# Kernel tuning notes

Measured on AMD Instinct MI355X. Metric: run time of the kernel, lower is better.

## Reference

```python
import jax, jax.numpy as jnp
import numpy as np

B, T, D, H = 4, 2048, 1024, 16
DK = D // H
LN_EPS = 1e-5


def setup_inputs() -> dict:
    key = jax.random.key(0)
    ks = jax.random.split(key, 12)
    s = 1.0 / np.sqrt(D)
    inp = {
        'x': jax.random.normal(ks[0], (B, T, D), jnp.float32),
        'Wq': jax.random.normal(ks[1], (D, D), jnp.float32) * s,
        'bq': jnp.zeros((D,), jnp.float32),
        'Wk': jax.random.normal(ks[2], (D, D), jnp.float32) * s,
        'bk': jnp.zeros((D,), jnp.float32),
        'Wv': jax.random.normal(ks[3], (D, D), jnp.float32) * s,
        'bv': jnp.zeros((D,), jnp.float32),
        'Wo': jax.random.normal(ks[4], (D, D), jnp.float32) * s,
        'bo': jnp.zeros((D,), jnp.float32),
        'ln_g': jnp.ones((D,), jnp.float32),
        'ln_b': jnp.zeros((D,), jnp.float32),
    }
    return inp


def reference(x, Wq, bq, Wk, bk, Wv, bv, Wo, bo, ln_g, ln_b):
    b, t, d = x.shape
    scale = jnp.sqrt(jnp.asarray(DK, x.dtype))
    # QKV projections -> [b, h, t, dk]
    q = (x @ Wq + bq).reshape(b, t, H, DK).transpose(0, 2, 1, 3)
    k = (x @ Wk + bk).reshape(b, t, H, DK).transpose(0, 2, 1, 3)
    v = (x @ Wv + bv).reshape(b, t, H, DK).transpose(0, 2, 1, 3)
    scores = jnp.einsum('bhqd,bhkd->bhqk', q, k) / scale  # [b,h,t,t]
    mask = jnp.tril(jnp.ones((t, t), x.dtype))[None, None]  # [1,1,t,t]
    neg = jnp.finfo(x.dtype).min
    scores = jnp.where(mask == 0, neg, scores)
    attn = jax.nn.softmax(scores, axis=-1)
    # mask-renormalize (as in the torch module)
    attn = attn * mask
    denom = attn.sum(-1, keepdims=True)
    attn = jnp.where(denom > 0, attn / denom, jnp.zeros_like(attn))
    ctx = jnp.einsum('bhqk,bhkd->bhqd', attn, v)  # [b,h,t,dk]
    ctx = ctx.transpose(0, 2, 1, 3).reshape(b, t, d)
    out = ctx @ Wo + bo
    y = out + x  # residual
    mu = y.mean(-1, keepdims=True)
    var = ((y - mu) ** 2).mean(-1, keepdims=True)
    return (y - mu) / jnp.sqrt(var + LN_EPS) * ln_g + ln_b
```

## Files before the change

### kernel.cpp

```cpp
#include <hip/hip_runtime.h>


using u16 = unsigned short;
using u32 = unsigned int;
typedef _Float16 f16x8 __attribute__((ext_vector_type(8)));
typedef float f32x4 __attribute__((ext_vector_type(4)));
typedef unsigned short u16x8 __attribute__((ext_vector_type(8)));

template <bool B> struct BoolTag { static constexpr bool v = B; };

__device__ inline u16 f2h_bits(float f) {
    _Float16 h = (_Float16)f;
    return __builtin_bit_cast(u16, h);
}

__device__ __forceinline__ void gload16(const void* g, void* l) {
    __builtin_amdgcn_global_load_lds(
        (const __attribute__((address_space(1))) void*)g,
        (__attribute__((address_space(3))) void*)l, 16, 0, 0);
}

__global__ __launch_bounds__(256) void convert_x_kernel(const float* __restrict__ x,
                                                        u16* __restrict__ xb) {
    size_t i = ((size_t)blockIdx.x * 256 + threadIdx.x) * 8;
    float4 a = *(const float4*)(x + i);
    float4 b = *(const float4*)(x + i + 4);
    u16x8 o;
    o[0] = f2h_bits(a.x); o[1] = f2h_bits(a.y); o[2] = f2h_bits(a.z); o[3] = f2h_bits(a.w);
    o[4] = f2h_bits(b.x); o[5] = f2h_bits(b.y); o[6] = f2h_bits(b.z); o[7] = f2h_bits(b.w);
    *(u16x8*)(xb + i) = o;
}

__global__ __launch_bounds__(256) void convert_wt_kernel(const float* __restrict__ W,
                                                         u16* __restrict__ Wt) {
    __shared__ float ts[64][68];
    const int k0 = blockIdx.x * 64, n0 = blockIdx.y * 64;
    const int tid = threadIdx.x, rr = tid >> 3, c = tid & 7;
#pragma unroll
    for (int p = 0; p < 2; p++) {
        int k = p * 32 + rr;
        float4 u = *(const float4*)(W + (size_t)(k0 + k) * 1024 + n0 + c * 8);
        float4 w = *(const float4*)(W + (size_t)(k0 + k) * 1024 + n0 + c * 8 + 4);
        *(float4*)&ts[k][c * 8] = u;
        *(float4*)&ts[k][c * 8 + 4] = w;
    }
    __syncthreads();
#pragma unroll
    for (int p = 0; p < 2; p++) {
        int n = p * 32 + rr;
        u16 o[8];
#pragma unroll
        for (int j = 0; j < 8; j++) o[j] = f2h_bits(ts[c * 8 + j][n]);
        *(u16x8*)(Wt + (size_t)(n0 + n) * 1024 + k0 + c * 8) = *(u16x8*)o;
    }
}

template <int MODE>
__global__ __launch_bounds__(512) void gemm256_kernel(
    const u16* __restrict__ A, const u16* __restrict__ Wt,
    const float* __restrict__ b0, const float* __restrict__ b1,
    const float* __restrict__ b2, u16* __restrict__ qo, u16* __restrict__ ko,
    u16* __restrict__ vo, float* __restrict__ outf,
    const float* __restrict__ xres) {
    constexpr int NBY = (MODE == 0) ? 12 : 4;
    __shared__ u16 As[3][128 * 64];
    __shared__ u16 Bs[3][256 * 64];

    const int bid = blockIdx.x;
    const int cpx = (MODE == 0) ? 96 : 32;
    const int swz = (bid & 7) * cpx + (bid >> 3);
    const int bx = swz / NBY, by = swz % NBY;
    const size_t row0 = (size_t)bx * 128;
    const size_t col0 = (size_t)by * 256;

    const int tid = threadIdx.x, lane = tid & 63;
    const int wid = tid >> 6, wm = wid >> 2, wn = wid & 3;
    const int l15 = lane & 15, lg = lane >> 4;
    const int rr = tid >> 3, c8 = tid & 7;
    const int scw = (c8 ^ (rr & 7)) * 8;

    f32x4 acc[4][4] = {};

    auto stage_half = [&](int kt, u16* dA, u16* dB, int h) {
        const int k0 = kt * 64;
        if (h == 0) {
            gload16(A + (row0 + rr) * 1024 + k0 + scw, dA + tid * 8);
            gload16(Wt + (col0 + rr) * 1024 + k0 + scw, dB + tid * 8);
            gload16(Wt + (col0 + 64 + rr) * 1024 + k0 + scw, dB + (512 + tid) * 8);
        } else {
            gload16(A + (row0 + 64 + rr) * 1024 + k0 + scw, dA + (512 + tid) * 8);
            gload16(Wt + (col0 + 128 + rr) * 1024 + k0 + scw, dB + (1024 + tid) * 8);
            gload16(Wt + (col0 + 192 + rr) * 1024 + k0 + scw, dB + (1536 + tid) * 8);
        }
    };

    auto ldops = [&](const u16* bA, const u16* bB, int kcv, f16x8* Af, f16x8* Bf) {
        const int swo = ((kcv * 4 + lg) ^ (l15 & 7)) * 8;
#pragma unroll
        for (int n = 0; n < 4; n++)
            Bf[n] = *(const f16x8*)(bB + (wn * 64 + n * 16 + l15) * 64 + swo);
#pragma unroll
        for (int m = 0; m < 4; m++)
            Af[m] = *(const f16x8*)(bA + (wm * 64 + m * 16 + l15) * 64 + swo);
    };

    auto domfma = [&](const f16x8* Af, const f16x8* Bf) {
        __builtin_amdgcn_s_setprio(1);
#pragma unroll
        for (int m = 0; m < 4; m++)
#pragma unroll
            for (int n = 0; n < 4; n++)
                acc[m][n] = __builtin_amdgcn_mfma_f32_16x16x32_f16(
                    Af[m], Bf[n], acc[m][n], 0, 0, 0);
        __builtin_amdgcn_s_setprio(0);
    };

    u16 *pA = &As[0][0], *pnA = &As[1][0], *ppA = &As[2][0];
    u16 *pB = &Bs[0][0], *pnB = &Bs[1][0], *ppB = &Bs[2][0];

    stage_half(0, pA, pB, 0);
    stage_half(0, pA, pB, 1);
    stage_half(1, pnA, pnB, 0);
    stage_half(1, pnA, pnB, 1);
    asm volatile("s_waitcnt vmcnt(6)" ::: "memory");
    __builtin_amdgcn_sched_barrier(0);
    __builtin_amdgcn_s_barrier();

#pragma unroll 1
    for (int t = 0; t < 16; t++) {
        f16x8 af[4], bf[4];
        ldops(pA, pB, 0, af, bf);
        if (t < 14) stage_half(t + 2, ppA, ppB, 0);
        __builtin_amdgcn_sched_barrier(0);
        __builtin_amdgcn_s_barrier();
        asm volatile("s_waitcnt lgkmcnt(0)" ::: "memory");
        __builtin_amdgcn_sched_barrier(0);
        domfma(af, bf);
        __builtin_amdgcn_sched_barrier(0);
        __builtin_amdgcn_s_barrier();
        ldops(pA, pB, 1, af, bf);
        if (t < 14) stage_half(t + 2, ppA, ppB, 1);
        if (t < 14)       asm volatile("s_waitcnt vmcnt(6)" ::: "memory");
        else if (t == 14) asm volatile("s_waitcnt vmcnt(0)" ::: "memory");
        __builtin_amdgcn_sched_barrier(0);
        __builtin_amdgcn_s_barrier();
        asm volatile("s_waitcnt lgkmcnt(0)" ::: "memory");
        __builtin_amdgcn_sched_barrier(0);
        domfma(af, bf);
        __builtin_amdgcn_sched_barrier(0);
        if (t < 15) {
            __builtin_amdgcn_s_barrier();
            u16* tp;
            tp = pA; pA = pnA; pnA = ppA; ppA = tp;
            tp = pB; pB = pnB; pnB = ppB; ppB = tp;
        }
    }

    if (MODE == 0) {
        const int zsel = by >> 2;
        u16* ob = zsel == 0 ? qo : (zsel == 1 ? ko : vo);
        const float* bias = zsel == 0 ? b0 : (zsel == 1 ? b1 : b2);
        const float qs = zsel == 0 ? 0.18033688f : 1.0f;
#pragma unroll
        for (int m = 0; m < 4; m++) {
#pragma unroll
            for (int n = 0; n < 4; n++) {
                size_t col = col0 + wn * 64 + n * 16 + l15;
                size_t colz = col & 1023;
                float bb = bias[colz];
#pragma unroll
                for (int r = 0; r < 4; r++) {
                    size_t row = row0 + wm * 64 + m * 16 + lg * 4 + r;
                    ob[row * 1024 + colz] = f2h_bits((acc[m][n][r] + bb) * qs);
                }
            }
        }
    } else {
#pragma unroll
        for (int m = 0; m < 4; m++) {
#pragma unroll
            for (int n = 0; n < 4; n++) {
                size_t col = col0 + wn * 64 + n * 16 + l15;
                float bb = b0[col];
#pragma unroll
                for (int r = 0; r < 4; r++) {
                    size_t row = row0 + wm * 64 + m * 16 + lg * 4 + r;
                    size_t idx = row * 1024 + col;
                    outf[idx] = acc[m][n][r] + bb + xres[idx];
                }
            }
        }
    }
}

__global__ __launch_bounds__(256) void transpose_v_kernel(const u16* __restrict__ V,
                                                          u16* __restrict__ Vt) {
    __shared__ u16 ts[64][72];
    const int bh = blockIdx.y;
    const int b = bh >> 4, h = bh & 15;
    const int t0 = blockIdx.x * 64;
    const int tid = threadIdx.x, rr = tid >> 3, c = tid & 7;
#pragma unroll
    for (int p = 0; p < 2; p++) {
        int t = p * 32 + rr;
        *(u16x8*)&ts[t][c * 8] =
            *(const u16x8*)(V + ((size_t)b * 2048 + t0 + t) * 1024 + h * 64 + c * 8);
    }
    __syncthreads();
#pragma unroll
    for (int p = 0; p < 2; p++) {
        int d = p * 32 + rr;
        u16 o[8];
#pragma unroll
        for (int j = 0; j < 8; j++) o[j] = ts[c * 8 + j][d];
        *(u16x8*)(Vt + ((size_t)bh * 64 + d) * 2048 + t0 + c * 8) = *(u16x8*)o;
    }
}

__global__ __launch_bounds__(256) void attn_kernel(const u16* __restrict__ Q,
                                                   const u16* __restrict__ Kb,
                                                   const u16* __restrict__ Vt,
                                                   u16* __restrict__ ctx) {
    __shared__ u16 Ks[2][64 * 64];
    __shared__ u16 Vs[2][64 * 64];
    __shared__ u16 Ps[8][16 * 72];

    const int bh = blockIdx.x;
    const int b = bh >> 4, h = bh & 15;
    const int qb = 15 - (int)blockIdx.y;
    const int tid = threadIdx.x, lane = tid & 63, wid = tid >> 6;
    const int l15 = lane & 15, lg = lane >> 4;
    const int q0w = qb * 128 + wid * 32;
    const int send = qb * 128;

    const int rr = tid >> 3, c8 = tid & 7;
    const int scw = (c8 ^ (rr & 7)) * 8;
    const size_t kbase = ((size_t)b * 2048) * 1024 + h * 64 + scw;
    const size_t vbase = ((size_t)bh * 64 + rr) * 2048 + scw;

    f16x8 qv[2][2];
#pragma unroll
    for (int qf = 0; qf < 2; qf++) {
        size_t qoff = ((size_t)b * 2048 + q0w + qf * 16 + l15) * 1024 + h * 64 + lg * 8;
        qv[qf][0] = *(const f16x8*)(Q + qoff);
        qv[qf][1] = *(const f16x8*)(Q + qoff + 32);
    }

    const int swk0 = (lg ^ (l15 & 7)) * 8;
    const int swk1 = ((4 + lg) ^ (l15 & 7)) * 8;
    u16* Pw0 = Ps[wid * 2 + 0] + l15 * 72;
    u16* Pw1 = Ps[wid * 2 + 1] + l15 * 72;

    f32x4 acc[2][4] = {};
    float psum[2] = {0.0f, 0.0f};

    auto stage = [&](int s, int bf) {
#pragma unroll
        for (int ph = 0; ph < 2; ph++) {
            gload16(Kb + kbase + (size_t)(s + ph * 32 + rr) * 1024,
                    Ks[bf] + (ph * 256 + wid * 64) * 8);
            gload16(Vt + vbase + (size_t)(ph * 32) * 2048 + s,
                    Vs[bf] + (ph * 256 + wid * 64) * 8);
        }
    };

    auto body = [&](int s, int bf, auto maskc) {
        constexpr bool MASK = decltype(maskc)::v;
        f32x4 sc[2][4];
#pragma unroll
        for (int c = 0; c < 4; c++) {
            const u16* kp = Ks[bf] + (c * 16 + l15) * 64;
            f16x8 kf0 = *(const f16x8*)(kp + swk0);
            f16x8 kf1 = *(const f16x8*)(kp + swk1);
#pragma unroll
            for (int qf = 0; qf < 2; qf++) {
                f32x4 z = {};
                z = __builtin_amdgcn_mfma_f32_16x16x32_f16(kf0, qv[qf][0], z, 0, 0, 0);
                z = __builtin_amdgcn_mfma_f32_16x16x32_f16(kf1, qv[qf][1], z, 0, 0, 0);
                sc[qf][c] = z;
            }
        }
#pragma unroll
        for (int qf = 0; qf < 2; qf++) {
            u16* Pw = qf ? Pw1 : Pw0;
#pragma unroll
            for (int c = 0; c < 4; c++) {
                float pv[4];
#pragma unroll
                for (int r = 0; r < 4; r++) {
                    float e = __builtin_amdgcn_exp2f(fminf(sc[qf][c][r], 15.0f));
                    if (MASK) {
                        int kk = s + c * 16 + lg * 4 + r;
                        e = (kk <= q0w + qf * 16 + l15) ? e : 0.0f;
                    }
                    psum[qf] += e;
                    pv[r] = e;
                }
                uint2 w;
                w.x = __builtin_bit_cast(u32, __builtin_amdgcn_cvt_pkrtz(pv[0], pv[1]));
                w.y = __builtin_bit_cast(u32, __builtin_amdgcn_cvt_pkrtz(pv[2], pv[3]));
                *(uint2*)(Pw + c * 16 + lg * 4) = w;
            }
        }
        f16x8 pa0[2], pa1[2];
#pragma unroll
        for (int qf = 0; qf < 2; qf++) {
            const u16* Pw = qf ? Pw1 : Pw0;
            pa0[qf] = *(const f16x8*)(Pw + lg * 8);
            pa1[qf] = *(const f16x8*)(Pw + 32 + lg * 8);
        }
#pragma unroll
        for (int dt = 0; dt < 4; dt++) {
            const u16* vp = Vs[bf] + (dt * 16 + l15) * 64;
            f16x8 vf0 = *(const f16x8*)(vp + swk0);
            f16x8 vf1 = *(const f16x8*)(vp + swk1);
#pragma unroll
            for (int qf = 0; qf < 2; qf++) {
                acc[qf][dt] =
                    __builtin_amdgcn_mfma_f32_16x16x32_f16(pa0[qf], vf0, acc[qf][dt], 0, 0, 0);
                acc[qf][dt] =
                    __builtin_amdgcn_mfma_f32_16x16x32_f16(pa1[qf], vf1, acc[qf][dt], 0, 0, 0);
            }
        }
    };

    stage(0, 0);
    int cur = 0;
    for (int s = 0; s < send; s += 64) {
        __syncthreads();
        stage(s + 64, cur ^ 1);
        body(s, cur, BoolTag<false>{});
        cur ^= 1;
    }
    __syncthreads();
    stage(send + 64, cur ^ 1);
    body(send, cur, BoolTag<true>{});
    cur ^= 1;
    __syncthreads();
    if (wid >= 2) body(send + 64, cur, BoolTag<true>{});

#pragma unroll
    for (int qf = 0; qf < 2; qf++) {
        psum[qf] += __shfl_xor(psum[qf], 16);
        psum[qf] += __shfl_xor(psum[qf], 32);
    }
#pragma unroll
    for (int qf = 0; qf < 2; qf++) {
        float inv = 1.0f / psum[qf];
#pragma unroll
        for (int r = 0; r < 4; r++) {
            float ir = __shfl(inv, lg * 4 + r);
            size_t row = (size_t)b * 2048 + q0w + qf * 16 + lg * 4 + r;
#pragma unroll
            for (int dt = 0; dt < 4; dt++)
                ctx[row * 1024 + h * 64 + dt * 16 + l15] = f2h_bits(acc[qf][dt][r] * ir);
        }
    }
}

__global__ __launch_bounds__(256) void ln_kernel(const float* __restrict__ y,
                                                 const float* __restrict__ g,
                                                 const float* __restrict__ bb,
                                                 float* __restrict__ out) {
    const int r = blockIdx.x, tid = threadIdx.x;
    float4 v = *(const float4*)(y + (size_t)r * 1024 + tid * 4);
    float s = v.x + v.y + v.z + v.w;
    float sq = v.x * v.x + v.y * v.y + v.z * v.z + v.w * v.w;
#pragma unroll
    for (int ofs = 1; ofs < 64; ofs <<= 1) {
        s += __shfl_xor(s, ofs);
        sq += __shfl_xor(sq, ofs);
    }
    __shared__ float as[4], aq[4];
    if ((tid & 63) == 0) { as[tid >> 6] = s; aq[tid >> 6] = sq; }
    __syncthreads();
    s = as[0] + as[1] + as[2] + as[3];
    sq = aq[0] + aq[1] + aq[2] + aq[3];
    float mu = s * (1.0f / 1024.0f);
    float var = sq * (1.0f / 1024.0f) - mu * mu;
    float rstd = rsqrtf(var + 1e-5f);
    float4 gv = *(const float4*)(g + tid * 4);
    float4 bv = *(const float4*)(bb + tid * 4);
    float4 o4;
    o4.x = (v.x - mu) * rstd * gv.x + bv.x;
    o4.y = (v.y - mu) * rstd * gv.y + bv.y;
    o4.z = (v.z - mu) * rstd * gv.z + bv.z;
    o4.w = (v.w - mu) * rstd * gv.w + bv.w;
    *(float4*)(out + (size_t)r * 1024 + tid * 4) = o4;
}

extern "C" void kernel_launch(void* const* d_in, const int* in_sizes, int n_in,
                              void* d_out, int out_size, void* d_ws, size_t ws_size,
                              hipStream_t stream) {
    const float* x  = (const float*)d_in[0];
    const float* Wq = (const float*)d_in[1];
    const float* bq = (const float*)d_in[2];
    const float* Wk = (const float*)d_in[3];
    const float* bk = (const float*)d_in[4];
    const float* Wv = (const float*)d_in[5];
    const float* bv = (const float*)d_in[6];
    const float* Wo = (const float*)d_in[7];
    const float* bo = (const float*)d_in[8];
    const float* lg = (const float*)d_in[9];
    const float* lb = (const float*)d_in[10];
    float* out = (float*)d_out;

    char* ws = (char*)d_ws;
    u16* xb = (u16*)(ws + 0);
    u16* wt = (u16*)(ws + 16777216);
    u16* q  = (u16*)(ws + 25165824);
    u16* k  = (u16*)(ws + 41943040);
    u16* v  = (u16*)(ws + 58720256);
    u16* vt = (u16*)(ws + 75497472);
    u16* cx = (u16*)(ws + 92274688);
    float* y = (float*)(ws + 109051904);

    convert_x_kernel<<<4096, 256, 0, stream>>>(x, xb);
    dim3 gw(16, 16);
    convert_wt_kernel<<<gw, 256, 0, stream>>>(Wq, wt);
    convert_wt_kernel<<<gw, 256, 0, stream>>>(Wk, wt + 1048576);
    convert_wt_kernel<<<gw, 256, 0, stream>>>(Wv, wt + 2097152);
    convert_wt_kernel<<<gw, 256, 0, stream>>>(Wo, wt + 3145728);

    gemm256_kernel<0><<<768, 512, 0, stream>>>(xb, wt, bq, bk, bv, q, k, v,
                                               nullptr, nullptr);
    transpose_v_kernel<<<dim3(32, 64), 256, 0, stream>>>(v, vt);
    attn_kernel<<<dim3(64, 16), 256, 0, stream>>>(q, k, vt, cx);
    gemm256_kernel<1><<<256, 512, 0, stream>>>(cx, wt + 3145728, bo, nullptr,
                                               nullptr, nullptr, nullptr, nullptr,
                                               y, x);
    ln_kernel<<<8192, 256, 0, stream>>>(y, lg, lb, out);
}
```

Measured before the change: 200.2 us.

## Fuse V transpose into QKV GEMM epilogue and enlarge attention query tiles

The QKV GEMM epilogue now writes V transposed through shared memory straight into the Vt layout, so the separate transpose kernel and its extra pass over V are gone. The attention kernel doubles each workgroup's query tile to 256 rows (64 per wave), which halves the grid and reuses each staged K/V tile across more queries. Row sums of P are now computed with an MFMA against a vector of ones instead of scalar adds plus shuffles. The cost is more accumulator registers per wave, which may lower occupancy, a longer masked diagonal section, and fewer workgroups to spread the causal imbalance.

```diff
diff --git a/kernel.cpp b/kernel.cpp
--- a/kernel.cpp
+++ b/kernel.cpp
@@ -60,7 +60,7 @@
     const u16* __restrict__ A, const u16* __restrict__ Wt,
     const float* __restrict__ b0, const float* __restrict__ b1,
     const float* __restrict__ b2, u16* __restrict__ qo, u16* __restrict__ ko,
-    u16* __restrict__ vo, float* __restrict__ outf,
+    u16* __restrict__ vt, float* __restrict__ outf,
     const float* __restrict__ xres) {
     constexpr int NBY = (MODE == 0) ? 12 : 4;
     __shared__ u16 As[3][128 * 64];
@@ -158,22 +158,48 @@
 
     if (MODE == 0) {
         const int zsel = by >> 2;
-        u16* ob = zsel == 0 ? qo : (zsel == 1 ? ko : vo);
-        const float* bias = zsel == 0 ? b0 : (zsel == 1 ? b1 : b2);
-        const float qs = zsel == 0 ? 0.18033688f : 1.0f;
-#pragma unroll
-        for (int m = 0; m < 4; m++) {
-#pragma unroll
-            for (int n = 0; n < 4; n++) {
-                size_t col = col0 + wn * 64 + n * 16 + l15;
-                size_t colz = col & 1023;
-                float bb = bias[colz];
-#pragma unroll
-                for (int r = 0; r < 4; r++) {
-                    size_t row = row0 + wm * 64 + m * 16 + lg * 4 + r;
-                    ob[row * 1024 + colz] = f2h_bits((acc[m][n][r] + bb) * qs);
+        if (zsel < 2) {
+            u16* ob = zsel == 0 ? qo : ko;
+            const float* bias = zsel == 0 ? b0 : b1;
+            const float qs = zsel == 0 ? 0.18033688f : 1.0f;
+#pragma unroll
+            for (int m = 0; m < 4; m++) {
+#pragma unroll
+                for (int n = 0; n < 4; n++) {
+                    size_t col = col0 + wn * 64 + n * 16 + l15;
+                    size_t colz = col & 1023;
+                    float bb = bias[colz];
+#pragma unroll
+                    for (int r = 0; r < 4; r++) {
+                        size_t row = row0 + wm * 64 + m * 16 + lg * 4 + r;
+                        ob[row * 1024 + colz] = f2h_bits((acc[m][n][r] + bb) * qs);
+                    }
                 }
             }
+        } else {
+            u16* TL = &Bs[0][0];
+            __syncthreads();
+#pragma unroll
+            for (int m = 0; m < 4; m++) {
+#pragma unroll
+                for (int n = 0; n < 4; n++) {
+                    int cl = wn * 64 + n * 16 + l15;
+                    float bb = b2[(col0 & 1023) + cl];
+#pragma unroll
+                    for (int r = 0; r < 4; r++) {
+                        int rl = wm * 64 + m * 16 + lg * 4 + r;
+                        TL[cl * 136 + rl] = f2h_bits(acc[m][n][r] + bb);
+                    }
+                }
+            }
+            __syncthreads();
+            const int vrl = tid >> 1, th = tid & 1;
+            size_t vrow = (row0 >> 11) * 1024 + (col0 & 1023) + vrl;
+            const int t0loc = (int)(row0 & 2047) + th * 64;
+#pragma unroll
+            for (int j = 0; j < 8; j++)
+                *(u16x8*)(vt + vrow * 2048 + t0loc + j * 8) =
+                    *(const u16x8*)(TL + vrl * 136 + th * 64 + j * 8);
         }
     } else {
 #pragma unroll
@@ -193,54 +219,30 @@
     }
 }
 
-__global__ __launch_bounds__(256) void transpose_v_kernel(const u16* __restrict__ V,
-                                                          u16* __restrict__ Vt) {
-    __shared__ u16 ts[64][72];
-    const int bh = blockIdx.y;
-    const int b = bh >> 4, h = bh & 15;
-    const int t0 = blockIdx.x * 64;
-    const int tid = threadIdx.x, rr = tid >> 3, c = tid & 7;
-#pragma unroll
-    for (int p = 0; p < 2; p++) {
-        int t = p * 32 + rr;
-        *(u16x8*)&ts[t][c * 8] =
-            *(const u16x8*)(V + ((size_t)b * 2048 + t0 + t) * 1024 + h * 64 + c * 8);
-    }
-    __syncthreads();
-#pragma unroll
-    for (int p = 0; p < 2; p++) {
-        int d = p * 32 + rr;
-        u16 o[8];
-#pragma unroll
-        for (int j = 0; j < 8; j++) o[j] = ts[c * 8 + j][d];
-        *(u16x8*)(Vt + ((size_t)bh * 64 + d) * 2048 + t0 + c * 8) = *(u16x8*)o;
-    }
-}
-
 __global__ __launch_bounds__(256) void attn_kernel(const u16* __restrict__ Q,
                                                    const u16* __restrict__ Kb,
                                                    const u16* __restrict__ Vt,
                                                    u16* __restrict__ ctx) {
     __shared__ u16 Ks[2][64 * 64];
     __shared__ u16 Vs[2][64 * 64];
-    __shared__ u16 Ps[8][16 * 72];
+    __shared__ u16 Ps[4][4][16][68];
 
     const int bh = blockIdx.x;
     const int b = bh >> 4, h = bh & 15;
-    const int qb = 15 - (int)blockIdx.y;
+    const int qb = 7 - (int)blockIdx.y;
     const int tid = threadIdx.x, lane = tid & 63, wid = tid >> 6;
     const int l15 = lane & 15, lg = lane >> 4;
-    const int q0w = qb * 128 + wid * 32;
-    const int send = qb * 128;
+    const int q0w = qb * 256 + wid * 64;
+    const int send = qb * 256;
 
     const int rr = tid >> 3, c8 = tid & 7;
     const int scw = (c8 ^ (rr & 7)) * 8;
     const size_t kbase = ((size_t)b * 2048) * 1024 + h * 64 + scw;
     const size_t vbase = ((size_t)bh * 64 + rr) * 2048 + scw;
 
-    f16x8 qv[2][2];
-#pragma unroll
-    for (int qf = 0; qf < 2; qf++) {
+    f16x8 qv[4][2];
+#pragma unroll
+    for (int qf = 0; qf < 4; qf++) {
         size_t qoff = ((size_t)b * 2048 + q0w + qf * 16 + l15) * 1024 + h * 64 + lg * 8;
         qv[qf][0] = *(const f16x8*)(Q + qoff);
         qv[qf][1] = *(const f16x8*)(Q + qoff + 32);
@@ -248,11 +250,13 @@
 
     const int swk0 = (lg ^ (l15 & 7)) * 8;
     const int swk1 = ((4 + lg) ^ (l15 & 7)) * 8;
-    u16* Pw0 = Ps[wid * 2 + 0] + l15 * 72;
-    u16* Pw1 = Ps[wid * 2 + 1] + l15 * 72;
-
-    f32x4 acc[2][4] = {};
-    float psum[2] = {0.0f, 0.0f};
+
+    f16x8 ones;
+#pragma unroll
+    for (int j = 0; j < 8; j++) ones[j] = (_Float16)1.0f;
+
+    f32x4 acc[4][4] = {};
+    f32x4 accs[4] = {};
 
     auto stage = [&](int s, int bf) {
 #pragma unroll
@@ -266,46 +270,36 @@
 
     auto body = [&](int s, int bf, auto maskc) {
         constexpr bool MASK = decltype(maskc)::v;
-        f32x4 sc[2][4];
 #pragma unroll
         for (int c = 0; c < 4; c++) {
             const u16* kp = Ks[bf] + (c * 16 + l15) * 64;
             f16x8 kf0 = *(const f16x8*)(kp + swk0);
             f16x8 kf1 = *(const f16x8*)(kp + swk1);
 #pragma unroll
-            for (int qf = 0; qf < 2; qf++) {
+            for (int qf = 0; qf < 4; qf++) {
                 f32x4 z = {};
                 z = __builtin_amdgcn_mfma_f32_16x16x32_f16(kf0, qv[qf][0], z, 0, 0, 0);
                 z = __builtin_amdgcn_mfma_f32_16x16x32_f16(kf1, qv[qf][1], z, 0, 0, 0);
-                sc[qf][c] = z;
-            }
-        }
-#pragma unroll
-        for (int qf = 0; qf < 2; qf++) {
-            u16* Pw = qf ? Pw1 : Pw0;
-#pragma unroll
-            for (int c = 0; c < 4; c++) {
                 float pv[4];
 #pragma unroll
                 for (int r = 0; r < 4; r++) {
-                    float e = __builtin_amdgcn_exp2f(fminf(sc[qf][c][r], 15.0f));
+                    float e = __builtin_amdgcn_exp2f(fminf(z[r], 15.0f));
                     if (MASK) {
                         int kk = s + c * 16 + lg * 4 + r;
                         e = (kk <= q0w + qf * 16 + l15) ? e : 0.0f;
                     }
-                    psum[qf] += e;
                     pv[r] = e;
                 }
                 uint2 w;
                 w.x = __builtin_bit_cast(u32, __builtin_amdgcn_cvt_pkrtz(pv[0], pv[1]));
                 w.y = __builtin_bit_cast(u32, __builtin_amdgcn_cvt_pkrtz(pv[2], pv[3]));
-                *(uint2*)(Pw + c * 16 + lg * 4) = w;
+                *(uint2*)(&Ps[wid][qf][l15][0] + c * 16 + lg * 4) = w;
             }
         }
-        f16x8 pa0[2], pa1[2];
-#pragma unroll
-        for (int qf = 0; qf < 2; qf++) {
-            const u16* Pw = qf ? Pw1 : Pw0;
+        f16x8 pa0[4], pa1[4];
+#pragma unroll
+        for (int qf = 0; qf < 4; qf++) {
+            const u16* Pw = &Ps[wid][qf][l15][0];
             pa0[qf] = *(const f16x8*)(Pw + lg * 8);
             pa1[qf] = *(const f16x8*)(Pw + 32 + lg * 8);
         }
@@ -315,12 +309,17 @@
             f16x8 vf0 = *(const f16x8*)(vp + swk0);
             f16x8 vf1 = *(const f16x8*)(vp + swk1);
 #pragma unroll
-            for (int qf = 0; qf < 2; qf++) {
+            for (int qf = 0; qf < 4; qf++) {
                 acc[qf][dt] =
                     __builtin_amdgcn_mfma_f32_16x16x32_f16(pa0[qf], vf0, acc[qf][dt], 0, 0, 0);
                 acc[qf][dt] =
                     __builtin_amdgcn_mfma_f32_16x16x32_f16(pa1[qf], vf1, acc[qf][dt], 0, 0, 0);
             }
+        }
+#pragma unroll
+        for (int qf = 0; qf < 4; qf++) {
+            accs[qf] = __builtin_amdgcn_mfma_f32_16x16x32_f16(pa0[qf], ones, accs[qf], 0, 0, 0);
+            accs[qf] = __builtin_amdgcn_mfma_f32_16x16x32_f16(pa1[qf], ones, accs[qf], 0, 0, 0);
         }
     };
 
@@ -332,28 +331,23 @@
         body(s, cur, BoolTag<false>{});
         cur ^= 1;
     }
-    __syncthreads();
-    stage(send + 64, cur ^ 1);
-    body(send, cur, BoolTag<true>{});
-    cur ^= 1;
-    __syncthreads();
-    if (wid >= 2) body(send + 64, cur, BoolTag<true>{});
-
-#pragma unroll
-    for (int qf = 0; qf < 2; qf++) {
-        psum[qf] += __shfl_xor(psum[qf], 16);
-        psum[qf] += __shfl_xor(psum[qf], 32);
-    }
-#pragma unroll
-    for (int qf = 0; qf < 2; qf++) {
-        float inv = 1.0f / psum[qf];
+#pragma unroll 1
+    for (int j = 0; j < 4; j++) {
+        __syncthreads();
+        if (j < 3) stage(send + 64 * (j + 1), cur ^ 1);
+        body(send + 64 * j, cur, BoolTag<true>{});
+        cur ^= 1;
+    }
+
+#pragma unroll
+    for (int qf = 0; qf < 4; qf++) {
 #pragma unroll
         for (int r = 0; r < 4; r++) {
-            float ir = __shfl(inv, lg * 4 + r);
+            float inv = 1.0f / accs[qf][r];
             size_t row = (size_t)b * 2048 + q0w + qf * 16 + lg * 4 + r;
 #pragma unroll
             for (int dt = 0; dt < 4; dt++)
-                ctx[row * 1024 + h * 64 + dt * 16 + l15] = f2h_bits(acc[qf][dt][r] * ir);
+                ctx[row * 1024 + h * 64 + dt * 16 + l15] = f2h_bits(acc[qf][dt][r] * inv);
         }
     }
 }
@@ -410,7 +404,6 @@
     u16* wt = (u16*)(ws + 16777216);
     u16* q  = (u16*)(ws + 25165824);
     u16* k  = (u16*)(ws + 41943040);
-    u16* v  = (u16*)(ws + 58720256);
     u16* vt = (u16*)(ws + 75497472);
     u16* cx = (u16*)(ws + 92274688);
     float* y = (float*)(ws + 109051904);
@@ -422,10 +415,9 @@
     convert_wt_kernel<<<gw, 256, 0, stream>>>(Wv, wt + 2097152);
     convert_wt_kernel<<<gw, 256, 0, stream>>>(Wo, wt + 3145728);
 
-    gemm256_kernel<0><<<768, 512, 0, stream>>>(xb, wt, bq, bk, bv, q, k, v,
+    gemm256_kernel<0><<<768, 512, 0, stream>>>(xb, wt, bq, bk, bv, q, k, vt,
                                                nullptr, nullptr);
-    transpose_v_kernel<<<dim3(32, 64), 256, 0, stream>>>(v, vt);
-    attn_kernel<<<dim3(64, 16), 256, 0, stream>>>(q, k, vt, cx);
+    attn_kernel<<<dim3(64, 8), 256, 0, stream>>>(q, k, vt, cx);
     gemm256_kernel<1><<<256, 512, 0, stream>>>(cx, wt + 3145728, bo, nullptr,
                                                nullptr, nullptr, nullptr, nullptr,
                                                y, x);
```

Result: slower. 237.4 us (+18.6%).
